# Kernel tuning notes

Measured on AMD Instinct MI355X. Metric: run time of the kernel, lower is better.

The kernel has to match this reference:

```python
import jax, jax.numpy as jnp
import numpy as np
from jax import lax

B, IN_CH, OUT_CH, H, W = 32, 128, 256, 64, 64
STYLE_CH, TDIM, G = 512, 512, 32
GN_EPS, MOD_EPS = 1e-5, 1e-8
DN = ('NCHW', 'OIHW', 'NCHW')


def swish(x):
    return x * jax.nn.sigmoid(x)


def group_norm(x, gamma, beta):
    n, c, h, w = x.shape
    xr = x.reshape(n, G, c // G, h, w)
    mu = xr.mean(axis=(2, 3, 4), keepdims=True)
    var = xr.var(axis=(2, 3, 4), keepdims=True)
    xn = ((xr - mu) * lax.rsqrt(var + GN_EPS)).reshape(n, c, h, w)
    return xn * gamma[None, :, None, None] + beta[None, :, None, None]


def conv3x3(x, w, b):
    y = lax.conv_general_dilated(x, w, (1, 1), ((1, 1), (1, 1)), dimension_numbers=DN)
    return y + b[None, :, None, None]


def setup_inputs() -> dict:
    key = jax.random.key(0)
    ks = jax.random.split(key, 16)
    s = 0.05
    return {
        'x': jax.random.normal(ks[0], (B, IN_CH, H, W), jnp.float32),
        'temb': jax.random.normal(ks[1], (B, TDIM), jnp.float32),
        'style': jax.random.normal(ks[2], (B, STYLE_CH), jnp.float32),
        'gn1_g': jnp.ones((IN_CH,), jnp.float32),
        'gn1_b': jnp.zeros((IN_CH,), jnp.float32),
        'conv1_w': jax.random.normal(ks[3], (OUT_CH, IN_CH, 3, 3), jnp.float32) * s,
        'conv1_b': jnp.zeros((OUT_CH,), jnp.float32),
        'temb_w': jax.random.normal(ks[4], (OUT_CH, TDIM), jnp.float32) * s,
        'temb_b': jnp.zeros((OUT_CH,), jnp.float32),
        'gn2_g': jnp.ones((OUT_CH,), jnp.float32),
        'gn2_b': jnp.zeros((OUT_CH,), jnp.float32),
        'style_w': jax.random.normal(ks[5], (OUT_CH, STYLE_CH), jnp.float32) * s,
        'style_b': jnp.zeros((OUT_CH,), jnp.float32),
        'mod_w': jax.random.normal(ks[6], (OUT_CH, OUT_CH, 3, 3), jnp.float32) * s,
        'sc_w': jax.random.normal(ks[7], (OUT_CH, IN_CH, 1, 1), jnp.float32) * s,
        'sc_b': jnp.zeros((OUT_CH,), jnp.float32),
    }


def reference(x, temb, style, gn1_g, gn1_b, conv1_w, conv1_b, temb_w, temb_b,
              gn2_g, gn2_b, style_w, style_b, mod_w, sc_w, sc_b):
    # block1: GN -> Swish -> Conv3x3
    h = conv3x3(swish(group_norm(x, gn1_g, gn1_b)), conv1_w, conv1_b)
    # temb projection: Swish -> Linear, broadcast over HxW
    h = h + (swish(temb) @ temb_w.T + temb_b)[:, :, None, None]
    # block2: GN -> Swish -> Dropout(0) [identity]
    h = swish(group_norm(h, gn2_g, gn2_b))
    # modulated + demodulated per-sample conv (StyleGAN2-style)
    style2 = style @ style_w.T + style_b                       # (b, out_ch)
    wmod = mod_w[None] * (style2[:, None, :, None, None] + 1.0)  # (b, o, i, kh, kw)
    d = lax.rsqrt((wmod ** 2).sum(axis=(2, 3, 4), keepdims=True) + MOD_EPS)
    wmod = wmod * d
    conv1s = lambda xi, wi: lax.conv_general_dilated(
        xi[None], wi, (1, 1), ((1, 1), (1, 1)), dimension_numbers=DN)[0]
    h = jax.vmap(conv1s)(h, wmod)                              # per-sample conv
    # shortcut 1x1 conv (in_ch != out_ch)
    sc = lax.conv_general_dilated(x, sc_w, (1, 1), ((0, 0), (0, 0)), dimension_numbers=DN)
    sc = sc + sc_b[None, :, None, None]
    return h + sc
```

## Files before the change

kernel.cpp:

```cpp
#include <hip/hip_runtime.h>
#include <cstdint>

typedef unsigned short u16;
typedef unsigned int   u32;

typedef __attribute__((ext_vector_type(8))) short bf16x8;
typedef __attribute__((ext_vector_type(4))) float f32x4;

#define DEV __device__ __forceinline__

static constexpr int HP = 66, WP = 66;

DEV u16 f2bf(float f) {
  u32 u = __float_as_uint(f);
  u32 r = (u + 0x7fffu + ((u >> 16) & 1u)) >> 16;
  return (u16)r;
}
DEV float bf2f(u16 v) { return __uint_as_float((u32)v << 16); }

DEV void gload_lds16(const void* g, void* s) {
  __builtin_amdgcn_global_load_lds(
      (const __attribute__((address_space(1))) void*)g,
      (__attribute__((address_space(3))) void*)s, 16, 0, 0);
}

__global__ __launch_bounds__(256) void prep_kernel(const float* __restrict__ conv1_w,
                                                   const float* __restrict__ mod_w,
                                                   u16* __restrict__ w1T,
                                                   u16* __restrict__ wmT,
                                                   float* __restrict__ SS_T,
                                                   u16* __restrict__ act1p,
                                                   u16* __restrict__ act2p,
                                                   float* __restrict__ s2sum) {
  int blk = blockIdx.x, t = threadIdx.x;
  if (blk < 1152) {
    int idx = blk * 256 + t;
    int co = idx / 1152, r = idx - co * 1152;
    int s = r >> 7, ci = r & 127;
    int ky = s / 3, kx = s - ky * 3;
    w1T[idx] = f2bf(conv1_w[(co * 128 + ci) * 9 + ky * 3 + kx]);
  } else if (blk < 3456) {
    int idx = (blk - 1152) * 256 + t;
    int co = idx / 2304, r = idx - co * 2304;
    int s = r >> 8, ci = r & 255;
    int ky = s / 3, kx = s - ky * 3;
    wmT[idx] = f2bf(mod_w[(co * 256 + ci) * 9 + ky * 3 + kx]);
  } else if (blk < 3712) {
    int o = blk - 3456, i = t;
    const float* p = mod_w + (size_t)(o * 256 + i) * 9;
    float s = 0.f;
#pragma unroll
    for (int k = 0; k < 9; ++k) s += p[k] * p[k];
    SS_T[i * 256 + o] = s;
  } else if (blk < 5272) {
    bool big = blk >= 4232;
    int idx = (big ? (blk - 4232) : (blk - 3712)) * 256 + t;
    const int GR = big ? 32 : 16;
    int g = idx % GR;
    int p = (idx / GR) % 260;
    int b = idx / (GR * 260);
    int y, x;
    if (p < 66)       { y = 0;       x = p; }
    else if (p < 132) { y = 65;      x = p - 66; }
    else if (p < 196) { y = p - 131; x = 0; }
    else              { y = p - 195; x = 65; }
    uint4 z; z.x = 0; z.y = 0; z.z = 0; z.w = 0;
    u16* buf = big ? act2p : act1p;
    int C = big ? 256 : 128;
    *(uint4*)(buf + (((size_t)b * HP + y) * WP + x) * C + g * 8) = z;
  } else {
    *(float2*)(s2sum + t * 8)     = make_float2(0.f, 0.f);
    *(float2*)(s2sum + t * 8 + 2) = make_float2(0.f, 0.f);
    *(float2*)(s2sum + t * 8 + 4) = make_float2(0.f, 0.f);
    *(float2*)(s2sum + t * 8 + 6) = make_float2(0.f, 0.f);
  }
}

__global__ __launch_bounds__(256) void temb_style_kernel(const float* __restrict__ temb,
                                                         const float* __restrict__ temb_w,
                                                         const float* __restrict__ temb_b,
                                                         const float* __restrict__ conv1_b,
                                                         const float* __restrict__ style,
                                                         const float* __restrict__ style_w,
                                                         const float* __restrict__ style_b,
                                                         float* __restrict__ tb2,
                                                         float* __restrict__ mvec) {
  __shared__ float sw[512];
  int blk = blockIdx.x, t = threadIdx.x;
  if (blk < 32) {
    int b = blk;
    for (int k = t; k < 512; k += 256) {
      float v = temb[b * 512 + k];
      sw[k] = v / (1.f + __expf(-v));
    }
    __syncthreads();
    const float4* wr = (const float4*)(temb_w + t * 512);
    float acc = 0.f;
    for (int k = 0; k < 128; ++k) {
      float4 w4 = wr[k];
      acc += w4.x * sw[k*4] + w4.y * sw[k*4+1] + w4.z * sw[k*4+2] + w4.w * sw[k*4+3];
    }
    tb2[b * 256 + t] = acc + temb_b[t] + conv1_b[t];
  } else {
    int b = blk - 32;
    for (int k = t; k < 512; k += 256) sw[k] = style[b * 512 + k];
    __syncthreads();
    const float4* wr = (const float4*)(style_w + t * 512);
    float acc = 0.f;
    for (int k = 0; k < 128; ++k) {
      float4 w4 = wr[k];
      acc += w4.x * sw[k*4] + w4.y * sw[k*4+1] + w4.z * sw[k*4+2] + w4.w * sw[k*4+3];
    }
    mvec[b * 256 + t] = acc + style_b[t] + 1.f;
  }
}

__global__ __launch_bounds__(256) void demod_kernel(const float* __restrict__ mvec,
                                                    const float* __restrict__ SS_T,
                                                    float* __restrict__ dvec) {
  __shared__ float m2[256];
  int b = blockIdx.x, t = threadIdx.x;
  float mv = mvec[b * 256 + t];
  m2[t] = mv * mv;
  __syncthreads();
  float acc = 0.f;
  for (int i = 0; i < 256; ++i) acc += m2[i] * SS_T[i * 256 + t];
  dvec[b * 256 + t] = rsqrtf(acc + 1e-8f);
}

__global__ __launch_bounds__(256) void scale_sc_kernel(const float* __restrict__ sc_w,
                                                       const float* __restrict__ dvec,
                                                       u16* __restrict__ scTb) {
  int idx = blockIdx.x * 256 + threadIdx.x;
  int ci = idx & 127;
  int co = (idx >> 7) & 255;
  int b  = idx >> 15;
  scTb[idx] = f2bf(sc_w[co * 128 + ci] / dvec[b * 256 + co]);
}

__global__ __launch_bounds__(256) void gn1_stats_kernel(const float* __restrict__ x,
                                                        float2* __restrict__ st1) {
  int bg = blockIdx.x;
  const float4* p = (const float4*)(x + (size_t)bg * 16384);
  float s = 0.f, s2 = 0.f;
  for (int i = threadIdx.x; i < 4096; i += 256) {
    float4 v = p[i];
    s  += v.x + v.y + v.z + v.w;
    s2 += v.x*v.x + v.y*v.y + v.z*v.z + v.w*v.w;
  }
  for (int d = 32; d; d >>= 1) { s += __shfl_down(s, d); s2 += __shfl_down(s2, d); }
  __shared__ float red[2][4];
  if ((threadIdx.x & 63) == 0) { red[0][threadIdx.x >> 6] = s; red[1][threadIdx.x >> 6] = s2; }
  __syncthreads();
  if (threadIdx.x == 0) {
    s  = red[0][0] + red[0][1] + red[0][2] + red[0][3];
    s2 = red[1][0] + red[1][1] + red[1][2] + red[1][3];
    float mean = s / 16384.f;
    float var  = s2 / 16384.f - mean * mean;
    st1[bg] = make_float2(mean, rsqrtf(var + 1e-5f));
  }
}

__global__ __launch_bounds__(256) void gn1_apply_kernel(const float* __restrict__ x,
                                                        const float2* __restrict__ st1,
                                                        const float* __restrict__ g1,
                                                        const float* __restrict__ b1,
                                                        u16* __restrict__ act1p,
                                                        u16* __restrict__ xh) {
  __shared__ float xs[64][129];
  int blk = blockIdx.x;
  int b = blk >> 6, y = blk & 63;
  int t = threadIdx.x;
#pragma unroll 8
  for (int pass = 0; pass < 32; ++pass) {
    int c = pass * 4 + (t >> 6);
    xs[t & 63][c] = x[(((size_t)b * 128 + c) * 64 + y) * 64 + (t & 63)];
  }
  __syncthreads();
  const int cg = t & 15, c0 = cg * 8;
  float2 msA = st1[b * 32 + cg * 2];
  float2 msB = st1[b * 32 + cg * 2 + 1];
  float g1r[8], b1r[8];
#pragma unroll
  for (int e = 0; e < 8; ++e) { g1r[e] = g1[c0 + e]; b1r[e] = b1[c0 + e]; }
#pragma unroll
  for (int p = 0; p < 4; ++p) {
    int xi = p * 16 + (t >> 4);
    u16 outA[8], outX[8];
#pragma unroll
    for (int e = 0; e < 8; ++e) {
      float v = xs[xi][c0 + e];
      float2 ms = (e < 4) ? msA : msB;
      float vn = (v - ms.x) * ms.y * g1r[e] + b1r[e];
      float sw = vn / (1.f + __expf(-vn));
      outA[e] = f2bf(sw);
      outX[e] = f2bf(v);
    }
    *(uint4*)(act1p + (((size_t)b * HP + (y + 1)) * WP + (xi + 1)) * 128 + c0) =
        *(const uint4*)outA;
    *(uint4*)(xh + (((size_t)b * 64 + y) * 64 + xi) * 128 + c0) = *(const uint4*)outX;
  }
}

__global__ __launch_bounds__(256) void gn2_apply_kernel(const u16* __restrict__ h1,
                                                        const float* __restrict__ st2sum,
                                                        const float* __restrict__ g2,
                                                        const float* __restrict__ b2,
                                                        const float* __restrict__ mvec,
                                                        u16* __restrict__ act2p) {
  int idx = blockIdx.x * 256 + threadIdx.x;
  int gpix = idx >> 5;
  int gi = idx & 31;
  int c0 = gi * 8;
  int b = gpix >> 12, y = (gpix >> 6) & 63, x = gpix & 63;
  uint4 raw = *(const uint4*)(h1 + (size_t)gpix * 256 + c0);
  const u16* rs = (const u16*)&raw;
  float s  = st2sum[b * 64 + gi * 2];
  float s2 = st2sum[b * 64 + gi * 2 + 1];
  float mean = s / 32768.f;
  float rstd = rsqrtf(s2 / 32768.f - mean * mean + 1e-5f);
  const float* mv = mvec + b * 256 + c0;
  u16 outp[8];
#pragma unroll
  for (int e = 0; e < 8; ++e) {
    float v  = bf2f(rs[e]);
    float vn = (v - mean) * rstd * g2[c0 + e] + b2[c0 + e];
    float sw = vn / (1.f + __expf(-vn));
    outp[e] = f2bf(sw * mv[e]);
  }
  *(uint4*)(act2p + (((size_t)b * HP + (y + 1)) * WP + (x + 1)) * 256 + c0) = *(const uint4*)outp;
}

template <int MODE>
__global__ __launch_bounds__(512, 2) void igemm_kernel(const u16* __restrict__ act,
                                                       const u16* __restrict__ wT,
                                                       const float* __restrict__ epi,
                                                       const u16* __restrict__ xh,
                                                       const u16* __restrict__ scTb,
                                                       const float* __restrict__ sc_b,
                                                       u16* __restrict__ h1out,
                                                       float* __restrict__ fout,
                                                       float* __restrict__ st2sum) {
  constexpr int CIN    = (MODE == 0) ? 128 : 256;
  constexpr int NSUB   = CIN / 64;
  constexpr int KW     = CIN * 9;
  constexpr int NKMAIN = KW / 64;
  constexpr int NKT    = (MODE == 2) ? NKMAIN + 2 : NKMAIN;

  __shared__ __align__(16) unsigned char lds[131072];
  const int tid  = threadIdx.x;
  const int wave = tid >> 6, lane = tid & 63;
  const int wm = wave >> 2, wn = wave & 3;
  const int m_base = blockIdx.x * 256;
  const int bimg = m_base >> 12;
  const int ln = lane & 15, l4 = lane >> 4;

  const int srow = lane >> 3;
  const int glog = (lane & 7) ^ srow;

  u32 pixA[2][2], pixX[2][2], rowB[2][2], rowS[2][2];
#pragma unroll
  for (int j = 0; j < 2; ++j)
#pragma unroll
    for (int h = 0; h < 2; ++h) {
      int mlocal = (wave & 3) * 16 + j * 8 + srow + h * 64 + (wave >> 2) * 128;
      int m = m_base + mlocal;
      int y = (m >> 6) & 63, x = m & 63;
      pixA[j][h] = (u32)((bimg * HP + y) * WP + x) * CIN + glog * 8;
      if (MODE == 2) pixX[j][h] = (u32)m * 128 + glog * 8;
      int co = (wave >> 1) * 64 + h * 32 + (wave & 1) * 16 + j * 8 + srow;
      rowB[j][h] = (u32)co * KW + glog * 8;
      if (MODE == 2) rowS[j][h] = (u32)(bimg * 256 + co) * 128 + glog * 8;
    }

  f32x4 acc[8][4];
#pragma unroll
  for (int i = 0; i < 8; ++i)
#pragma unroll
    for (int j = 0; j < 4; ++j) acc[i][j] = (f32x4){0.f, 0.f, 0.f, 0.f};

  auto stageA = [&](int kt, int h, int buf) {
    unsigned char* dst = lds + buf * 65536 + h * 16384 + wave * 2048;
    if (MODE == 2 && kt >= NKMAIN) {
      u32 ko = (u32)(kt - NKMAIN) * 64;
      gload_lds16(xh + pixX[0][h] + ko, dst);
      gload_lds16(xh + pixX[1][h] + ko, dst + 1024);
    } else {
      int tap = kt / NSUB;
      int kin = (kt - tap * NSUB) * 64;
      int ky = tap / 3, kx = tap - ky * 3;
      u32 ko = (u32)((ky * WP + kx) * CIN + kin);
      gload_lds16(act + pixA[0][h] + ko, dst);
      gload_lds16(act + pixA[1][h] + ko, dst + 1024);
    }
  };
  auto stageB = [&](int kt, int g, int buf) {
    unsigned char* dst = lds + buf * 65536 + 32768 + g * 16384 + wave * 2048;
    if (MODE == 2 && kt >= NKMAIN) {
      u32 ko = (u32)(kt - NKMAIN) * 64;
      gload_lds16(scTb + rowS[0][g] + ko, dst);
      gload_lds16(scTb + rowS[1][g] + ko, dst + 1024);
    } else {
      u32 ko = (u32)kt * 64;
      gload_lds16(wT + rowB[0][g] + ko, dst);
      gload_lds16(wT + rowB[1][g] + ko, dst + 1024);
    }
  };

  bf16x8 af[8], bf[4];
  auto ldA = [&](int h, int buf) {
    const unsigned char* As = lds + buf * 65536;
#pragma unroll
    for (int f = 0; f < 4; ++f)
#pragma unroll
      for (int kk = 0; kk < 2; ++kk) {
        int lr = h * 128 + wm * 64 + f * 16 + ln;
        int gr = (kk * 4 + l4) ^ (lr & 7);
        af[f * 2 + kk] = *(const bf16x8*)(As + lr * 128 + gr * 16);
      }
  };
  auto ldB = [&](int g, int buf) {
    const unsigned char* Bs = lds + buf * 65536 + 32768;
#pragma unroll
    for (int f1 = 0; f1 < 2; ++f1)
#pragma unroll
      for (int kk = 0; kk < 2; ++kk) {
        int lr = g * 128 + wn * 32 + f1 * 16 + ln;
        int gr = (kk * 4 + l4) ^ (lr & 7);
        bf[f1 * 2 + kk] = *(const bf16x8*)(Bs + lr * 128 + gr * 16);
      }
  };
  auto mmac = [&](int h, int g) {
    __builtin_amdgcn_s_setprio(1);
#pragma unroll
    for (int f = 0; f < 4; ++f)
#pragma unroll
      for (int f1 = 0; f1 < 2; ++f1)
#pragma unroll
        for (int kk = 0; kk < 2; ++kk)
          acc[h * 4 + f][g * 2 + f1] = __builtin_amdgcn_mfma_f32_16x16x32_bf16(
              af[f * 2 + kk], bf[f1 * 2 + kk], acc[h * 4 + f][g * 2 + f1], 0, 0, 0);
    __builtin_amdgcn_s_setprio(0);
  };

#define PHASE_BAR() do { __builtin_amdgcn_sched_barrier(0); \
    __builtin_amdgcn_s_barrier(); __builtin_amdgcn_sched_barrier(0); } while (0)

  stageA(0, 0, 0); stageB(0, 0, 0); stageB(0, 1, 0); stageA(0, 1, 0);

#pragma unroll 2
  for (int kt = 0; kt < NKT - 1; ++kt) {
    const int cur = kt & 1, nxt = cur ^ 1;
    stageA(kt + 1, 0, nxt);
    asm volatile("s_waitcnt vmcnt(6)" ::: "memory");
    PHASE_BAR();
    ldB(0, cur); ldA(0, cur);
    mmac(0, 0);
    stageB(kt + 1, 0, nxt);
    asm volatile("s_waitcnt vmcnt(6)" ::: "memory");
    PHASE_BAR();
    ldB(1, cur);
    mmac(0, 1);
    stageB(kt + 1, 1, nxt);
    asm volatile("s_waitcnt vmcnt(6)" ::: "memory");
    PHASE_BAR();
    ldA(1, cur);
    mmac(1, 1);
    stageA(kt + 1, 1, nxt);
    PHASE_BAR();
    ldB(0, cur);
    mmac(1, 0);
  }
  {
    const int cur = (NKT - 1) & 1;
    asm volatile("s_waitcnt vmcnt(4)" ::: "memory");
    PHASE_BAR();
    ldB(0, cur); ldA(0, cur); mmac(0, 0);
    asm volatile("s_waitcnt vmcnt(2)" ::: "memory");
    PHASE_BAR();
    ldB(1, cur); mmac(0, 1);
    asm volatile("s_waitcnt vmcnt(0)" ::: "memory");
    PHASE_BAR();
    ldA(1, cur); mmac(1, 1);
    PHASE_BAR();
    ldB(0, cur); mmac(1, 0);
  }
#undef PHASE_BAR

  if (MODE == 0) {
    const float* tbrow = epi + bimg * 256;
    float ps[4], ps2[4];
#pragma unroll
    for (int fn = 0; fn < 4; ++fn) { ps[fn] = 0.f; ps2[fn] = 0.f; }
#pragma unroll
    for (int fm = 0; fm < 8; ++fm)
#pragma unroll
      for (int fn = 0; fn < 4; ++fn) {
        int co = wn * 64 + fn * 16 + ln;
        float add = tbrow[co];
#pragma unroll
        for (int i = 0; i < 4; ++i) {
          int m = m_base + wm * 128 + fm * 16 + (l4 << 2) + i;
          float v = acc[fm][fn][i] + add;
          h1out[(size_t)m * 256 + co] = f2bf(v);
          ps[fn] += v; ps2[fn] += v * v;
        }
      }
#pragma unroll
    for (int fn = 0; fn < 4; ++fn) {
      float s = ps[fn], s2 = ps2[fn];
      s += __shfl_xor(s, 1);  s2 += __shfl_xor(s2, 1);
      s += __shfl_xor(s, 2);  s2 += __shfl_xor(s2, 2);
      s += __shfl_xor(s, 4);  s2 += __shfl_xor(s2, 4);
      s += __shfl_xor(s, 16); s2 += __shfl_xor(s2, 16);
      s += __shfl_xor(s, 32); s2 += __shfl_xor(s2, 32);
      if ((lane & 55) == 0) {
        int g = wn * 8 + fn * 2 + (ln >> 3);
        atomicAdd(&st2sum[bimg * 64 + g * 2 + 0], s);
        atomicAdd(&st2sum[bimg * 64 + g * 2 + 1], s2);
      }
    }
  } else {
    float* tile = (float*)lds;
    const int pixb = m_base & 4095;
#pragma unroll
    for (int c = 0; c < 4; ++c) {
      __syncthreads();
      if (wn == c) {
#pragma unroll
        for (int fn = 0; fn < 4; ++fn) {
          int nl = fn * 16 + ln;
          int co = c * 64 + nl;
          float dsc = epi[bimg * 256 + co];
          float scb = sc_b[co];
#pragma unroll
          for (int fm = 0; fm < 8; ++fm)
#pragma unroll
            for (int i = 0; i < 4; ++i) {
              int ml = wm * 128 + fm * 16 + (l4 << 2) + i;
              tile[nl * 257 + ml] = acc[fm][fn][i] * dsc + scb;
            }
        }
      }
      __syncthreads();
#pragma unroll 4
      for (int it = 0; it < 32; ++it) {
        int lin = it * 512 + tid;
        int co_l = lin >> 8, ml = lin & 255;
        fout[((size_t)(bimg * 256 + c * 64 + co_l)) * 4096 + pixb + ml] =
            tile[co_l * 257 + ml];
      }
    }
  }
}

extern "C" void kernel_launch(void* const* d_in, const int* in_sizes, int n_in,
                              void* d_out, int out_size, void* d_ws, size_t ws_size,
                              hipStream_t stream) {
  const float* x       = (const float*)d_in[0];
  const float* temb    = (const float*)d_in[1];
  const float* style   = (const float*)d_in[2];
  const float* gn1_g   = (const float*)d_in[3];
  const float* gn1_b   = (const float*)d_in[4];
  const float* conv1_w = (const float*)d_in[5];
  const float* conv1_b = (const float*)d_in[6];
  const float* temb_w  = (const float*)d_in[7];
  const float* temb_b  = (const float*)d_in[8];
  const float* gn2_g   = (const float*)d_in[9];
  const float* gn2_b   = (const float*)d_in[10];
  const float* style_w = (const float*)d_in[11];
  const float* style_b = (const float*)d_in[12];
  const float* mod_w   = (const float*)d_in[13];
  const float* sc_w    = (const float*)d_in[14];
  const float* sc_b    = (const float*)d_in[15];
  float* out = (float*)d_out;
  char* ws = (char*)d_ws;

  size_t o = 0;
  auto alloc = [&](size_t bytes) { size_t r = o; o += (bytes + 255) & ~(size_t)255; return r; };
  const size_t act1p_bytes = (size_t)32 * HP * WP * 128 * 2;
  const size_t xh_bytes    = (size_t)32 * 64 * 64 * 128 * 2;
  const size_t h1_bytes    = (size_t)32 * 4096 * 256 * 2;
  const size_t act2p_bytes = (size_t)32 * HP * WP * 256 * 2;
  size_t o_act1p = alloc(act1p_bytes);
  size_t o_xh    = alloc(xh_bytes);
  size_t o_h1    = alloc(h1_bytes);
  size_t o_act2p = alloc(act2p_bytes);
  size_t o_w1T   = alloc((size_t)256 * 1152 * 2);
  size_t o_wmT   = alloc((size_t)256 * 2304 * 2);
  size_t o_scTb  = alloc((size_t)32 * 256 * 128 * 2);
  size_t o_tb2   = alloc(8192 * 4);
  size_t o_mvec  = alloc(8192 * 4);
  size_t o_dvec  = alloc(8192 * 4);
  size_t o_SS    = alloc((size_t)256 * 256 * 4);
  size_t o_st1   = alloc(1024 * 8);
  size_t o_s2sum = alloc(32 * 32 * 2 * 4);
  if (ws_size < o) return;

  u16*    act1p = (u16*)(ws + o_act1p);
  u16*    xh    = (u16*)(ws + o_xh);
  u16*    h1    = (u16*)(ws + o_h1);
  u16*    act2p = (u16*)(ws + o_act2p);
  u16*    w1T   = (u16*)(ws + o_w1T);
  u16*    wmT   = (u16*)(ws + o_wmT);
  u16*    scTb  = (u16*)(ws + o_scTb);
  float*  tb2   = (float*)(ws + o_tb2);
  float*  mvec  = (float*)(ws + o_mvec);
  float*  dvec  = (float*)(ws + o_dvec);
  float*  SS_T  = (float*)(ws + o_SS);
  float2* st1   = (float2*)(ws + o_st1);
  float*  s2sum = (float*)(ws + o_s2sum);

  prep_kernel<<<5273, 256, 0, stream>>>(conv1_w, mod_w, w1T, wmT, SS_T,
                                        act1p, act2p, s2sum);
  temb_style_kernel<<<64, 256, 0, stream>>>(temb, temb_w, temb_b, conv1_b,
                                            style, style_w, style_b, tb2, mvec);
  gn1_stats_kernel<<<1024, 256, 0, stream>>>(x, st1);
  gn1_apply_kernel<<<2048, 256, 0, stream>>>(x, st1, gn1_g, gn1_b, act1p, xh);
  demod_kernel<<<32, 256, 0, stream>>>(mvec, SS_T, dvec);
  scale_sc_kernel<<<4096, 256, 0, stream>>>(sc_w, dvec, scTb);

  igemm_kernel<0><<<512, 512, 0, stream>>>(act1p, w1T, tb2, nullptr, nullptr,
                                           nullptr, h1, nullptr, s2sum);

  gn2_apply_kernel<<<16384, 256, 0, stream>>>(h1, s2sum, gn2_g, gn2_b, mvec, act2p);

  igemm_kernel<2><<<512, 512, 0, stream>>>(act2p, wmT, dvec, xh, scTb,
                                           sc_b, nullptr, out, nullptr);
}
```

Before: 340.7 us.

## Merge small prep kernels into fewer launches and vectorize GN1 transpose loads

Folds the GN1 statistics and temb/style projections into the prep kernel, and fuses the demodulation and shortcut-weight scaling into one kernel. This drops the launch count from nine to six and cuts small-kernel gaps and tail effects. The GN1 apply kernel now loads x with float4 reads instead of scalar loads, which may increase LDS bank conflicts on the transposed store. The fused demod_sc kernel runs only 32 blocks, each writing 128 values per thread, so that phase has little parallelism.

```diff
diff --git a/kernel.cpp b/kernel.cpp
--- a/kernel.cpp
+++ b/kernel.cpp
@@ -24,50 +24,108 @@
       (__attribute__((address_space(3))) void*)s, 16, 0, 0);
 }
 
-__global__ __launch_bounds__(256) void prep_kernel(const float* __restrict__ conv1_w,
+__global__ __launch_bounds__(256) void prep_kernel(const float* __restrict__ x,
+                                                   const float* __restrict__ temb,
+                                                   const float* __restrict__ temb_w,
+                                                   const float* __restrict__ temb_b,
+                                                   const float* __restrict__ conv1_b,
+                                                   const float* __restrict__ style,
+                                                   const float* __restrict__ style_w,
+                                                   const float* __restrict__ style_b,
+                                                   const float* __restrict__ conv1_w,
                                                    const float* __restrict__ mod_w,
+                                                   float2* __restrict__ st1,
+                                                   float* __restrict__ tb2,
+                                                   float* __restrict__ mvec,
                                                    u16* __restrict__ w1T,
                                                    u16* __restrict__ wmT,
                                                    float* __restrict__ SS_T,
                                                    u16* __restrict__ act1p,
                                                    u16* __restrict__ act2p,
                                                    float* __restrict__ s2sum) {
+  __shared__ float sh[512];
   int blk = blockIdx.x, t = threadIdx.x;
-  if (blk < 1152) {
-    int idx = blk * 256 + t;
+  if (blk < 1024) {
+    const float4* p = (const float4*)(x + (size_t)blk * 16384);
+    float s = 0.f, s2 = 0.f;
+    for (int i = t; i < 4096; i += 256) {
+      float4 v = p[i];
+      s  += v.x + v.y + v.z + v.w;
+      s2 += v.x*v.x + v.y*v.y + v.z*v.z + v.w*v.w;
+    }
+    for (int d = 32; d; d >>= 1) { s += __shfl_down(s, d); s2 += __shfl_down(s2, d); }
+    if ((t & 63) == 0) { sh[t >> 6] = s; sh[4 + (t >> 6)] = s2; }
+    __syncthreads();
+    if (t == 0) {
+      s  = sh[0] + sh[1] + sh[2] + sh[3];
+      s2 = sh[4] + sh[5] + sh[6] + sh[7];
+      float mean = s / 16384.f;
+      float var  = s2 / 16384.f - mean * mean;
+      st1[blk] = make_float2(mean, rsqrtf(var + 1e-5f));
+    }
+  } else if (blk < 1088) {
+    int b2 = blk - 1024;
+    if (b2 < 32) {
+      int b = b2;
+      for (int k = t; k < 512; k += 256) {
+        float v = temb[b * 512 + k];
+        sh[k] = v / (1.f + __expf(-v));
+      }
+      __syncthreads();
+      const float4* wr = (const float4*)(temb_w + t * 512);
+      float acc = 0.f;
+      for (int k = 0; k < 128; ++k) {
+        float4 w4 = wr[k];
+        acc += w4.x * sh[k*4] + w4.y * sh[k*4+1] + w4.z * sh[k*4+2] + w4.w * sh[k*4+3];
+      }
+      tb2[b * 256 + t] = acc + temb_b[t] + conv1_b[t];
+    } else {
+      int b = b2 - 32;
+      for (int k = t; k < 512; k += 256) sh[k] = style[b * 512 + k];
+      __syncthreads();
+      const float4* wr = (const float4*)(style_w + t * 512);
+      float acc = 0.f;
+      for (int k = 0; k < 128; ++k) {
+        float4 w4 = wr[k];
+        acc += w4.x * sh[k*4] + w4.y * sh[k*4+1] + w4.z * sh[k*4+2] + w4.w * sh[k*4+3];
+      }
+      mvec[b * 256 + t] = acc + style_b[t] + 1.f;
+    }
+  } else if (blk < 2240) {
+    int idx = (blk - 1088) * 256 + t;
     int co = idx / 1152, r = idx - co * 1152;
     int s = r >> 7, ci = r & 127;
     int ky = s / 3, kx = s - ky * 3;
     w1T[idx] = f2bf(conv1_w[(co * 128 + ci) * 9 + ky * 3 + kx]);
-  } else if (blk < 3456) {
-    int idx = (blk - 1152) * 256 + t;
+  } else if (blk < 4544) {
+    int idx = (blk - 2240) * 256 + t;
     int co = idx / 2304, r = idx - co * 2304;
     int s = r >> 8, ci = r & 255;
     int ky = s / 3, kx = s - ky * 3;
     wmT[idx] = f2bf(mod_w[(co * 256 + ci) * 9 + ky * 3 + kx]);
-  } else if (blk < 3712) {
-    int o = blk - 3456, i = t;
+  } else if (blk < 4800) {
+    int o = blk - 4544, i = t;
     const float* p = mod_w + (size_t)(o * 256 + i) * 9;
     float s = 0.f;
 #pragma unroll
     for (int k = 0; k < 9; ++k) s += p[k] * p[k];
     SS_T[i * 256 + o] = s;
-  } else if (blk < 5272) {
-    bool big = blk >= 4232;
-    int idx = (big ? (blk - 4232) : (blk - 3712)) * 256 + t;
+  } else if (blk < 6360) {
+    bool big = blk >= 5320;
+    int idx = (big ? (blk - 5320) : (blk - 4800)) * 256 + t;
     const int GR = big ? 32 : 16;
     int g = idx % GR;
     int p = (idx / GR) % 260;
     int b = idx / (GR * 260);
-    int y, x;
-    if (p < 66)       { y = 0;       x = p; }
-    else if (p < 132) { y = 65;      x = p - 66; }
-    else if (p < 196) { y = p - 131; x = 0; }
-    else              { y = p - 195; x = 65; }
+    int y, x2;
+    if (p < 66)       { y = 0;       x2 = p; }
+    else if (p < 132) { y = 65;      x2 = p - 66; }
+    else if (p < 196) { y = p - 131; x2 = 0; }
+    else              { y = p - 195; x2 = 65; }
     uint4 z; z.x = 0; z.y = 0; z.z = 0; z.w = 0;
     u16* buf = big ? act2p : act1p;
     int C = big ? 256 : 128;
-    *(uint4*)(buf + (((size_t)b * HP + y) * WP + x) * C + g * 8) = z;
+    *(uint4*)(buf + (((size_t)b * HP + y) * WP + x2) * C + g * 8) = z;
   } else {
     *(float2*)(s2sum + t * 8)     = make_float2(0.f, 0.f);
     *(float2*)(s2sum + t * 8 + 2) = make_float2(0.f, 0.f);
@@ -76,48 +134,11 @@
   }
 }
 
-__global__ __launch_bounds__(256) void temb_style_kernel(const float* __restrict__ temb,
-                                                         const float* __restrict__ temb_w,
-                                                         const float* __restrict__ temb_b,
-                                                         const float* __restrict__ conv1_b,
-                                                         const float* __restrict__ style,
-                                                         const float* __restrict__ style_w,
-                                                         const float* __restrict__ style_b,
-                                                         float* __restrict__ tb2,
-                                                         float* __restrict__ mvec) {
-  __shared__ float sw[512];
-  int blk = blockIdx.x, t = threadIdx.x;
-  if (blk < 32) {
-    int b = blk;
-    for (int k = t; k < 512; k += 256) {
-      float v = temb[b * 512 + k];
-      sw[k] = v / (1.f + __expf(-v));
-    }
-    __syncthreads();
-    const float4* wr = (const float4*)(temb_w + t * 512);
-    float acc = 0.f;
-    for (int k = 0; k < 128; ++k) {
-      float4 w4 = wr[k];
-      acc += w4.x * sw[k*4] + w4.y * sw[k*4+1] + w4.z * sw[k*4+2] + w4.w * sw[k*4+3];
-    }
-    tb2[b * 256 + t] = acc + temb_b[t] + conv1_b[t];
-  } else {
-    int b = blk - 32;
-    for (int k = t; k < 512; k += 256) sw[k] = style[b * 512 + k];
-    __syncthreads();
-    const float4* wr = (const float4*)(style_w + t * 512);
-    float acc = 0.f;
-    for (int k = 0; k < 128; ++k) {
-      float4 w4 = wr[k];
-      acc += w4.x * sw[k*4] + w4.y * sw[k*4+1] + w4.z * sw[k*4+2] + w4.w * sw[k*4+3];
-    }
-    mvec[b * 256 + t] = acc + style_b[t] + 1.f;
-  }
-}
-
-__global__ __launch_bounds__(256) void demod_kernel(const float* __restrict__ mvec,
-                                                    const float* __restrict__ SS_T,
-                                                    float* __restrict__ dvec) {
+__global__ __launch_bounds__(256) void demod_sc_kernel(const float* __restrict__ mvec,
+                                                       const float* __restrict__ SS_T,
+                                                       const float* __restrict__ sc_w,
+                                                       float* __restrict__ dvec,
+                                                       u16* __restrict__ scTb) {
   __shared__ float m2[256];
   int b = blockIdx.x, t = threadIdx.x;
   float mv = mvec[b * 256 + t];
@@ -125,39 +146,17 @@
   __syncthreads();
   float acc = 0.f;
   for (int i = 0; i < 256; ++i) acc += m2[i] * SS_T[i * 256 + t];
-  dvec[b * 256 + t] = rsqrtf(acc + 1e-8f);
-}
-
-__global__ __launch_bounds__(256) void scale_sc_kernel(const float* __restrict__ sc_w,
-                                                       const float* __restrict__ dvec,
-                                                       u16* __restrict__ scTb) {
-  int idx = blockIdx.x * 256 + threadIdx.x;
-  int ci = idx & 127;
-  int co = (idx >> 7) & 255;
-  int b  = idx >> 15;
-  scTb[idx] = f2bf(sc_w[co * 128 + ci] / dvec[b * 256 + co]);
-}
-
-__global__ __launch_bounds__(256) void gn1_stats_kernel(const float* __restrict__ x,
-                                                        float2* __restrict__ st1) {
-  int bg = blockIdx.x;
-  const float4* p = (const float4*)(x + (size_t)bg * 16384);
-  float s = 0.f, s2 = 0.f;
-  for (int i = threadIdx.x; i < 4096; i += 256) {
-    float4 v = p[i];
-    s  += v.x + v.y + v.z + v.w;
-    s2 += v.x*v.x + v.y*v.y + v.z*v.z + v.w*v.w;
-  }
-  for (int d = 32; d; d >>= 1) { s += __shfl_down(s, d); s2 += __shfl_down(s2, d); }
-  __shared__ float red[2][4];
-  if ((threadIdx.x & 63) == 0) { red[0][threadIdx.x >> 6] = s; red[1][threadIdx.x >> 6] = s2; }
-  __syncthreads();
-  if (threadIdx.x == 0) {
-    s  = red[0][0] + red[0][1] + red[0][2] + red[0][3];
-    s2 = red[1][0] + red[1][1] + red[1][2] + red[1][3];
-    float mean = s / 16384.f;
-    float var  = s2 / 16384.f - mean * mean;
-    st1[bg] = make_float2(mean, rsqrtf(var + 1e-5f));
+  float X = acc + 1e-8f;
+  dvec[b * 256 + t] = rsqrtf(X);
+  float invd = sqrtf(X);
+  const float4* wr = (const float4*)(sc_w + t * 128);
+  u16* dst = scTb + ((size_t)b * 256 + t) * 128;
+#pragma unroll 8
+  for (int c4 = 0; c4 < 32; ++c4) {
+    float4 w4 = wr[c4];
+    u16 o[4] = { f2bf(w4.x * invd), f2bf(w4.y * invd),
+                 f2bf(w4.z * invd), f2bf(w4.w * invd) };
+    *(uint2*)(dst + c4 * 4) = *(const uint2*)o;
   }
 }
 
@@ -171,10 +170,15 @@
   int blk = blockIdx.x;
   int b = blk >> 6, y = blk & 63;
   int t = threadIdx.x;
-#pragma unroll 8
-  for (int pass = 0; pass < 32; ++pass) {
-    int c = pass * 4 + (t >> 6);
-    xs[t & 63][c] = x[(((size_t)b * 128 + c) * 64 + y) * 64 + (t & 63)];
+#pragma unroll
+  for (int pass = 0; pass < 8; ++pass) {
+    int c = pass * 16 + (t >> 4);
+    int k = t & 15;
+    float4 v = *(const float4*)(x + ((size_t)(b * 128 + c)) * 4096 + y * 64 + k * 4);
+    xs[k * 4 + 0][c] = v.x;
+    xs[k * 4 + 1][c] = v.y;
+    xs[k * 4 + 2][c] = v.z;
+    xs[k * 4 + 3][c] = v.w;
   }
   __syncthreads();
   const int cg = t & 15, c0 = cg * 8;
@@ -511,14 +515,12 @@
   float2* st1   = (float2*)(ws + o_st1);
   float*  s2sum = (float*)(ws + o_s2sum);
 
-  prep_kernel<<<5273, 256, 0, stream>>>(conv1_w, mod_w, w1T, wmT, SS_T,
+  prep_kernel<<<6361, 256, 0, stream>>>(x, temb, temb_w, temb_b, conv1_b,
+                                        style, style_w, style_b, conv1_w, mod_w,
+                                        st1, tb2, mvec, w1T, wmT, SS_T,
                                         act1p, act2p, s2sum);
-  temb_style_kernel<<<64, 256, 0, stream>>>(temb, temb_w, temb_b, conv1_b,
-                                            style, style_w, style_b, tb2, mvec);
-  gn1_stats_kernel<<<1024, 256, 0, stream>>>(x, st1);
   gn1_apply_kernel<<<2048, 256, 0, stream>>>(x, st1, gn1_g, gn1_b, act1p, xh);
-  demod_kernel<<<32, 256, 0, stream>>>(mvec, SS_T, dvec);
-  scale_sc_kernel<<<4096, 256, 0, stream>>>(sc_w, dvec, scTb);
+  demod_sc_kernel<<<32, 256, 0, stream>>>(mvec, SS_T, sc_w, dvec, scTb);
 
   igemm_kernel<0><<<512, 512, 0, stream>>>(act1p, w1T, tb2, nullptr, nullptr,
                                            nullptr, h1, nullptr, s2sum);
```

After: 344.0 us. About the same (+1.0%).
